# Kernel optimization log

Measured on AMD Instinct MI355X. Metric: run time of the kernel, lower is better.

The kernel has to match this reference:

```python
import jax, jax.numpy as jnp
import numpy as np

B, S, D = 2, 2048, 1024   # batch, seq, d_model
E, K, H = 8, 4, 1024      # experts, top-k, expert hidden
SH = 2 * H                # shared-expert hidden (n_shared_experts=2)


def setup_inputs() -> dict:
    key = jax.random.key(0)
    ks = jax.random.split(key, 24)
    f = lambda k, shape: jax.random.normal(k, shape, dtype=jnp.float32) * 0.02
    return {
        "x": jax.random.normal(ks[0], (B, S, D), dtype=jnp.float32),
        # Linear(in_features, out_features), stored as [in, out]
        "lin0_w": f(ks[1], (D, D)), "lin0_b": f(ks[2], (D,)),
        "swi1_w1": f(ks[3], (D, D)), "swi1_b1": f(ks[4], (D,)),
        "swi1_w2": f(ks[5], (D, D)), "swi1_b2": f(ks[6], (D,)),
        # MoE router (no bias) + routed experts (SwiGLU FFN, no bias)
        "gate_w": f(ks[7], (E, D)),
        "exp_w1": f(ks[8], (E, D, H)),
        "exp_w3": f(ks[9], (E, D, H)),
        "exp_w2": f(ks[10], (E, H, D)),
        # shared experts fused into one wider SwiGLU MLP (2 shared experts)
        "sh_w1": f(ks[11], (D, SH)),
        "sh_w3": f(ks[12], (D, SH)),
        "sh_w2": f(ks[13], (SH, D)),
        # second Linear + SwiGLU block (num_ff=2)
        "lin1_w": f(ks[14], (D, D)), "lin1_b": f(ks[15], (D,)),
        "swi2_w1": f(ks[16], (D, D)), "swi2_b1": f(ks[17], (D,)),
        "swi2_w2": f(ks[18], (D, D)), "swi2_b2": f(ks[19], (D,)),
    }


def _silu(x):
    return x * jax.nn.sigmoid(x)


def _swiglu(x, w1, b1, w2, b2):
    return _silu(x @ w1 + b1) * (x @ w2 + b2)


def _moe(x, gate_w, exp_w1, exp_w3, exp_w2, sh_w1, sh_w3, sh_w2):
    b, s, d = x.shape
    t = b * s
    xt = x.reshape(t, d)
    # router: softmax scores, greedy top-k, normalized weights (scaling factor = 1)
    scores = jax.nn.softmax(xt @ gate_w.T, axis=-1)          # [T, E]
    topv, topi = jax.lax.top_k(scores, K)                    # [T, K]
    topv = topv / jnp.sum(topv, axis=-1, keepdims=True)
    combine = jnp.zeros((t, E), xt.dtype).at[jnp.arange(t)[:, None], topi].set(topv)  # [T, E]
    # routed experts: SwiGLU FFN per expert, dense-masked combine (same math as dispatch)
    g = _silu(jnp.einsum('td,edh->eth', xt, exp_w1))
    u = jnp.einsum('td,edh->eth', xt, exp_w3)
    yexp = jnp.einsum('eth,ehd->etd', g * u, exp_w2)         # [E, T, D]
    routed = jnp.einsum('te,etd->td', combine, yexp)         # [T, D]
    # shared experts (always on)
    shared = (_silu(xt @ sh_w1) * (xt @ sh_w3)) @ sh_w2      # [T, D]
    return (routed + shared).reshape(b, s, d)


def reference(x, lin0_w, lin0_b, swi1_w1, swi1_b1, swi1_w2, swi1_b2,
              gate_w, exp_w1, exp_w3, exp_w2, sh_w1, sh_w3, sh_w2,
              lin1_w, lin1_b, swi2_w1, swi2_b1, swi2_w2, swi2_b2):
    h = x @ lin0_w + lin0_b
    h = _swiglu(h, swi1_w1, swi1_b1, swi1_w2, swi1_b2)
    h = _moe(h, gate_w, exp_w1, exp_w3, exp_w2, sh_w1, sh_w3, sh_w2)
    h = h @ lin1_w + lin1_b
    h = _swiglu(h, swi2_w1, swi2_b1, swi2_w2, swi2_b2)
    return h
```

## Files before the change

### kernel.cpp

```cpp
#include <hip/hip_runtime.h>
#include <cstdint>
#include <cstddef>

#define T_TOKENS 4096
#define D_MODEL  1024
#define N_EXP    8
#define TOP_K    4
#define H_EXP    1024
#define SH_HID   2048
#define TK       (T_TOKENS*TOP_K)

typedef __bf16 bf16x8 __attribute__((ext_vector_type(8)));
typedef __bf16 bf16x4 __attribute__((ext_vector_type(4)));
typedef float  f32x4  __attribute__((ext_vector_type(4)));

__device__ __forceinline__ float silu_f(float x) {
    return x / (1.0f + expf(-x));
}

__device__ __forceinline__ void gload16(void* lds, const void* g)
{
    __builtin_amdgcn_global_load_lds(
        (const __attribute__((address_space(1))) unsigned int*)g,
        (__attribute__((address_space(3))) unsigned int*)lds,
        16, 0, 0);
}

template<int NT, bool SEG, bool GATHER, bool GLU>
__global__ __launch_bounds__(256)
void gemm_sp(const float* __restrict__ A, int lda,
             const float* __restrict__ W1, const float* __restrict__ W3,
             int64_t w_estride, int ldw,
             const float* __restrict__ bias1, const float* __restrict__ bias2,
             float* __restrict__ C, __bf16* __restrict__ Cb1, int ldc,
             int M, int Kd,
             const int* __restrict__ seg_off,
             const int* __restrict__ gather)
{
    constexpr int BM = 128, BN = 128, BK = 32;
    __shared__ __bf16 Asl[NT][BM * BK];
    __shared__ __bf16 Bsl[NT][BN * BK];

    int m0, m1, e = 0;
    if (SEG) {
        e = blockIdx.z;
        int s0 = seg_off[e], s1 = seg_off[e + 1];
        m0 = s0 + blockIdx.y * BM;
        if (m0 >= s1) return;
        m1 = (m0 + BM < s1) ? (m0 + BM) : s1;
    } else {
        m0 = blockIdx.y * BM;
        m1 = (m0 + BM < M) ? (m0 + BM) : M;
    }
    const int n0 = blockIdx.x * BN;

    const int tid  = threadIdx.x;
    const int lane = tid & 63;
    const int w    = tid >> 6;
    const int wm   = w >> 1, wn = w & 1;
    const int fr   = lane & 15, fq = lane >> 4;

    const float* aP[4]; int aR[4], aQ[4];
#pragma unroll
    for (int i = 0; i < 4; ++i) {
        int Li = tid + 256 * i;
        int r = Li >> 3, q = Li & 7;
        aR[i] = r; aQ[i] = q;
        int grow = m0 + r;
        if (grow > m1 - 1) grow = m1 - 1;
        if (GATHER) grow = gather[grow];
        aP[i] = A + (int64_t)grow * lda + q * 4;
    }

    const int bn  = tid & 127;
    const int bkh = tid >> 7;
    const float* Wsrc; int wcol;
    if (GLU) {
        int cl = n0 + bn;
// ... 121 lines not shown
                }
                if (NT == 3) {
                    a = __builtin_amdgcn_mfma_f32_16x16x32_bf16(af[1], bfr[1][jn], a, 0, 0, 0);
                    a = __builtin_amdgcn_mfma_f32_16x16x32_bf16(af[0], bfr[2][jn], a, 0, 0, 0);
                    a = __builtin_amdgcn_mfma_f32_16x16x32_bf16(af[2], bfr[0][jn], a, 0, 0, 0);
                }
                acc[im][jn] = a;
            }
        }
    }
#undef GLOADS

    if (GLU) {
#pragma unroll
        for (int jn = 0; jn < 4; jn += 2) {
            int gcol = (n0 >> 1) + wn * 32 + (jn >> 1) * 16 + fr;
            float bv1 = bias1 ? bias1[gcol] : 0.f;
            float bv2 = bias2 ? bias2[gcol] : 0.f;
#pragma unroll
            for (int im = 0; im < 4; ++im) {
                f32x4 v1 = acc[im][jn];
                f32x4 v2 = acc[im][jn + 1];
#pragma unroll
                for (int r = 0; r < 4; ++r) {
                    int grow = m0 + wm * 64 + im * 16 + fq * 4 + r;
                    if (grow < m1) {
                        float val = silu_f(v1[r] + bv1) * (v2[r] + bv2);
                        int64_t o = (int64_t)grow * ldc + gcol;
                        C[o] = val;
                        if (Cb1) Cb1[o] = (__bf16)val;
                    }
                }
            }
        }
    } else {
#pragma unroll
        for (int jn = 0; jn < 4; ++jn) {
            int col = n0 + wn * 64 + jn * 16 + fr;
            float bv = bias1 ? bias1[col] : 0.f;
#pragma unroll
            for (int im = 0; im < 4; ++im) {
                f32x4 v = acc[im][jn];
#pragma unroll
                for (int r = 0; r < 4; ++r) {
                    int grow = m0 + wm * 64 + im * 16 + fq * 4 + r;
                    if (grow < m1)
                        C[(int64_t)grow * ldc + col] = v[r] + bv;
                }
            }
        }
    }
}

template<bool SEG, bool GATHER, bool GLU, bool EMITB>
__global__ __launch_bounds__(256)
void gemm_gl(const __bf16* __restrict__ A, int lda,
             const __bf16* __restrict__ W1, const __bf16* __restrict__ W3,
             int64_t w_estride, int ldw,
             const float* __restrict__ bias1, const float* __restrict__ bias2,
             float* __restrict__ C, __bf16* __restrict__ Cb, int ldc,
             int M, int Kd,
             const int* __restrict__ seg_off,
             const int* __restrict__ gather)
{
    constexpr int BK = 32;
    __shared__ __bf16 Asl[2][128 * BK];
    __shared__ __bf16 Bsl[2][128 * BK];

    int m0, m1, e = 0;
    if (SEG) {
        e = blockIdx.z;
        int s0 = seg_off[e], s1 = seg_off[e + 1];
        m0 = s0 + blockIdx.y * 128;
        if (m0 >= s1) return;
        m1 = (m0 + 128 < s1) ? (m0 + 128) : s1;
    } else {
        m0 = blockIdx.y * 128;
        m1 = (m0 + 128 < M) ? (m0 + 128) : M;
    }
    const int n0 = blockIdx.x * 128;

    const int tid  = threadIdx.x;
    const int lane = tid & 63;
    const int w    = tid >> 6;
    const int wm   = w >> 1, wn = w & 1;
    const int fr   = lane & 15, fq = lane >> 4;

    const __bf16* As[2]; const __bf16* Ws[2];
    int ldsOff[2];
#pragma unroll
    for (int i = 0; i < 2; ++i) {
        int L = tid + 256 * i;
        int r = L >> 2, cp = L & 3;
        int cs = cp ^ ((r >> 1) & 3);
        ldsOff[i] = (i * 256 + w * 64) * 8;
        int grow = m0 + r;
        if (grow > m1 - 1) grow = m1 - 1;
        if (GATHER) grow = gather[grow];
        As[i] = A + (int64_t)grow * lda + cs * 8;
        int cl = n0 + r;
        const __bf16* base; int srcrow;
        if (GLU) {
            int B = cl >> 4;
            base = (B & 1) ? W3 : W1;
            srcrow = ((B >> 1) << 4) | (cl & 15);
        } else {
            base = W1; srcrow = cl;
        }
        Ws[i] = base + (int64_t)e * w_estride + (int64_t)srcrow * ldw + cs * 8;
    }

#define STAGE(buf, K0)                                                      \
    do {                                                                    \
        _Pragma("unroll")                                                   \
        for (int i = 0; i < 2; ++i) {                                       \
            gload16(&Asl[buf][ldsOff[i]], As[i] + (K0));                    \
            gload16(&Bsl[buf][ldsOff[i]], Ws[i] + (K0));                    \
        }                                                                   \
    } while (0)

    f32x4 zero4 = {0.f, 0.f, 0.f, 0.f};
    f32x4 acc[4][4];
#pragma unroll
    for (int i = 0; i < 4; ++i)
#pragma unroll
        for (int j = 0; j < 4; ++j) acc[i][j] = zero4;

    const int nk = Kd / BK;
    int cur = 0;
    STAGE(0, 0);
    __syncthreads();

    for (int ks = 0; ks < nk; ++ks) {
        if (ks + 1 < nk) STAGE(cur ^ 1, (ks + 1) * BK);

        bf16x8 bfr[4];
#pragma unroll
        for (int j = 0; j < 4; ++j) {
            int rown = wn * 64 + j * 16 + fr;
            int c = fq ^ ((rown >> 1) & 3);
            bfr[j] = *reinterpret_cast<const bf16x8*>(&Bsl[cur][rown * BK + c * 8]);
        }
#pragma unroll
        for (int im = 0; im < 4; ++im) {
            int rowm = wm * 64 + im * 16 + fr;
            int c = fq ^ ((rowm >> 1) & 3);
            bf16x8 af = *reinterpret_cast<const bf16x8*>(&Asl[cur][rowm * BK + c * 8]);
#pragma unroll
            for (int jn = 0; jn < 4; ++jn)
                acc[im][jn] = __builtin_amdgcn_mfma_f32_16x16x32_bf16(af, bfr[jn], acc[im][jn], 0, 0, 0);
        }
        __syncthreads();
        cur ^= 1;
    }
#undef STAGE

    if (GLU) {
#pragma unroll
        for (int jn = 0; jn < 4; jn += 2) {
            int gcol = (n0 >> 1) + wn * 32 + (jn >> 1) * 16 + fr;
            float bv1 = bias1 ? bias1[gcol] : 0.f;
            float bv2 = bias2 ? bias2[gcol] : 0.f;
#pragma unroll
            for (int im = 0; im < 4; ++im) {
                f32x4 v1 = acc[im][jn];
                f32x4 v2 = acc[im][jn + 1];
#pragma unroll
                for (int r = 0; r < 4; ++r) {
                    int grow = m0 + wm * 64 + im * 16 + fq * 4 + r;
                    if (grow < m1) {
                        float val = silu_f(v1[r] + bv1) * (v2[r] + bv2);
                        int64_t o = (int64_t)grow * ldc + gcol;
                        if (EMITB) Cb[o] = (__bf16)val;
                        else       C[o]  = val;
                    }
                }
            }
        }
    } else {
#pragma unroll
        for (int jn = 0; jn < 4; ++jn) {
            int col = n0 + wn * 64 + jn * 16 + fr;
            float bv = bias1 ? bias1[col] : 0.f;
#pragma unroll
            for (int im = 0; im < 4; ++im) {
                f32x4 v = acc[im][jn];
#pragma unroll
                for (int r = 0; r < 4; ++r) {
                    int grow = m0 + wm * 64 + im * 16 + fq * 4 + r;
                    if (grow < m1) {
                        int64_t o = (int64_t)grow * ldc + col;
                        if (EMITB) Cb[o] = (__bf16)(v[r] + bv);
                        else       C[o]  = v[r] + bv;
                    }
                }
            }
        }
    }
}

template<bool WBF, bool SEG, bool GATHER, bool GLU, bool EMITB>
__global__ __launch_bounds__(256)
void gemm_bb(const __bf16* __restrict__ A, int lda,
             const void* __restrict__ W1v, const void* __restrict__ W3v,
             int64_t w_estride, int ldw,
             const float* __restrict__ bias1, const float* __restrict__ bias2,
             float* __restrict__ C, __bf16* __restrict__ Cb, int ldc,
             int M, int Kd,
             const int* __restrict__ seg_off,
             const int* __restrict__ gather)
{
    constexpr int BK = 32;
    __shared__ __bf16 Asl[128 * BK];
    __shared__ __bf16 Bsl[128 * BK];

    int m0, m1, e = 0;
    if (SEG) {
        e = blockIdx.z;
        int s0 = seg_off[e], s1 = seg_off[e + 1];
        m0 = s0 + blockIdx.y * 128;
        if (m0 >= s1) return;
        m1 = (m0 + 128 < s1) ? (m0 + 128) : s1;
    } else {
        m0 = blockIdx.y * 128;
        m1 = (m0 + 128 < M) ? (m0 + 128) : M;
    }
    const int n0 = blockIdx.x * 128;

    const int tid  = threadIdx.x;
    const int lane = tid & 63;
    const int w    = tid >> 6;
    const int wm   = w >> 1, wn = w & 1;
    const int fr   = lane & 15, fq = lane >> 4;

    int aWr[2]; const __bf16* Ab[2];
#pragma unroll
    for (int i = 0; i < 2; ++i) {
        int L = tid + 256 * i;
        int r = L >> 2, ch = L & 3;
        aWr[i] = r * BK + (ch ^ ((r >> 1) & 3)) * 8;
        int grow = m0 + r;
        if (grow > m1 - 1) grow = m1 - 1;
        if (GATHER) grow = gather[grow];
        Ab[i] = A + (int64_t)grow * lda + ch * 8;
    }

    const int bn  = tid & 127;
    const int bkh = tid >> 7;
    int wcol; const void* Wsel;
    if (GLU) {
        int cl = n0 + bn;
        int B  = cl >> 4;
        Wsel = (B & 1) ? W3v : W1v;
        wcol = ((B >> 1) << 4) | (cl & 15);
    } else {
        Wsel = W1v; wcol = n0 + bn;
    }
    const float* Wbf = (const float*)Wsel + (int64_t)e * w_estride + (int64_t)(bkh * 16) * ldw + wcol;
    int wWrS[2];
#pragma unroll
    for (int c = 0; c < 2; ++c)
        wWrS[c] = bn * BK + ((bkh * 2 + c) ^ ((bn >> 1) & 3)) * 8;

    f32x4 zero4 = {0.f, 0.f, 0.f, 0.f};
    f32x4 acc[4][4];
#pragma unroll
    for (int i = 0; i < 4; ++i)
#pragma unroll
        for (int j = 0; j < 4; ++j) acc[i][j] = zero4;

    bf16x8 areg[2];
    bf16x8 wreg[2];

#define GLOADS(K0)                                                          \
    do {                                                                    \
        areg[0] = *reinterpret_cast<const bf16x8*>(Ab[0] + (K0));           \
        areg[1] = *reinterpret_cast<const bf16x8*>(Ab[1] + (K0));           \
        _Pragma("unroll")                                                   \
        for (int j = 0; j < 16; ++j)                                        \
            wreg[j >> 3][j & 7] = (__bf16)Wbf[(int64_t)((K0) + j) * ldw];   \
    } while (0)

    const int nk = Kd / BK;
    GLOADS(0);

    for (int ks = 0; ks < nk; ++ks) {
        __syncthreads();
        *reinterpret_cast<bf16x8*>(&Asl[aWr[0]]) = areg[0];
        *reinterpret_cast<bf16x8*>(&Asl[aWr[1]]) = areg[1];
        *reinterpret_cast<bf16x8*>(&Bsl[wWrS[0]]) = wreg[0];
        *reinterpret_cast<bf16x8*>(&Bsl[wWrS[1]]) = wreg[1];
        if (ks + 1 < nk) GLOADS((ks + 1) * BK);
        __syncthreads();

        bf16x8 bfr[4];
#pragma unroll
        for (int j = 0; j < 4; ++j) {
            int rown = wn * 64 + j * 16 + fr;
            int c = fq ^ ((rown >> 1) & 3);
            bfr[j] = *reinterpret_cast<const bf16x8*>(&Bsl[rown * BK + c * 8]);
        }
#pragma unroll
        for (int im = 0; im < 4; ++im) {
            int rowm = wm * 64 + im * 16 + fr;
            int c = fq ^ ((rowm >> 1) & 3);
            bf16x8 af = *reinterpret_cast<const bf16x8*>(&Asl[rowm * BK + c * 8]);
#pragma unroll
            for (int jn = 0; jn < 4; ++jn)
                acc[im][jn] = __builtin_amdgcn_mfma_f32_16x16x32_bf16(af, bfr[jn], acc[im][jn], 0, 0, 0);
        }
    }
#undef GLOADS

    if (GLU) {
#pragma unroll
        for (int jn = 0; jn < 4; jn += 2) {
            int gcol = (n0 >> 1) + wn * 32 + (jn >> 1) * 16 + fr;
            float bv1 = bias1 ? bias1[gcol] : 0.f;
            float bv2 = bias2 ? bias2[gcol] : 0.f;
#pragma unroll
            for (int im = 0; im < 4; ++im) {
                f32x4 v1 = acc[im][jn];
                f32x4 v2 = acc[im][jn + 1];
#pragma unroll
                for (int r = 0; r < 4; ++r) {
                    int grow = m0 + wm * 64 + im * 16 + fq * 4 + r;
                    if (grow < m1) {
                        float val = silu_f(v1[r] + bv1) * (v2[r] + bv2);
                        int64_t o = (int64_t)grow * ldc + gcol;
                        if (EMITB) Cb[o] = (__bf16)val;
                        else       C[o]  = val;
                    }
                }
            }
        }
    } else {
#pragma unroll
        for (int jn = 0; jn < 4; ++jn) {
            int col = n0 + wn * 64 + jn * 16 + fr;
            float bv = bias1 ? bias1[col] : 0.f;
#pragma unroll
            for (int im = 0; im < 4; ++im) {
                f32x4 v = acc[im][jn];
#pragma unroll
                for (int r = 0; r < 4; ++r) {
                    int grow = m0 + wm * 64 + im * 16 + fq * 4 + r;
                    if (grow < m1) {
                        int64_t o = (int64_t)grow * ldc + col;
                        if (EMITB) Cb[o] = (__bf16)(v[r] + bv);
                        else       C[o]  = v[r] + bv;
                    }
                }
            }
        }
    }
}

__global__ __launch_bounds__(256)
void f2bT(const float* __restrict__ src, __bf16* __restrict__ dst, int R, int C)
{
    __shared__ float t[32][33];
    const int64_t eoff = (int64_t)blockIdx.z * R * C;
    src += eoff; dst += eoff;
    const int c0 = blockIdx.x * 32, r0 = blockIdx.y * 32;
    const int tx = threadIdx.x & 31, ty = threadIdx.x >> 5;
#pragma unroll
    for (int i = 0; i < 4; ++i) {
        int r = r0 + ty + i * 8;
        t[ty + i * 8][tx] = src[(int64_t)r * C + c0 + tx];
    }
    __syncthreads();
#pragma unroll
    for (int i = 0; i < 4; ++i) {
        int c = c0 + ty + i * 8;
        dst[(int64_t)c * R + r0 + tx] = (__bf16)t[tx][ty + i * 8];
    }
}

__global__ __launch_bounds__(256)
void router_logits(const float* __restrict__ h1, const float* __restrict__ gw,
                   int* __restrict__ topi, float* __restrict__ topw,
                   unsigned char* __restrict__ emask)
{
    const int wave = threadIdx.x >> 6, lane = threadIdx.x & 63;
    const int t = blockIdx.x * 4 + wave;
    const float* x = h1 + (int64_t)t * D_MODEL;
    float part[N_EXP];
#pragma unroll
    for (int e = 0; e < N_EXP; ++e) part[e] = 0.f;
#pragma unroll 4
    for (int i = 0; i < D_MODEL / 64; ++i) {
        int d = lane + 64 * i;
        float xv = x[d];
#pragma unroll
        for (int e = 0; e < N_EXP; ++e)
            part[e] = fmaf(xv, gw[e * D_MODEL + d], part[e]);
    }
#pragma unroll
    for (int m = 32; m > 0; m >>= 1)
#pragma unroll
        for (int e = 0; e < N_EXP; ++e)
            part[e] += __shfl_xor(part[e], m, 64);

    if (lane == 0) {
        float p[N_EXP];
        float mx = -1e30f;
#pragma unroll
        for (int e = 0; e < N_EXP; ++e) mx = part[e] > mx ? part[e] : mx;
        float z = 0.f;
#pragma unroll
        for (int e = 0; e < N_EXP; ++e) { p[e] = expf(part[e] - mx); z += p[e]; }
#pragma unroll
        for (int e = 0; e < N_EXP; ++e) p[e] /= z;
        bool used[N_EXP];
#pragma unroll
        for (int e = 0; e < N_EXP; ++e) used[e] = false;
        int sel[TOP_K]; float sv[TOP_K]; float wsum = 0.f;
        unsigned m8 = 0;
        for (int k = 0; k < TOP_K; ++k) {
            int best = 0; float bvv = -1.f;
            for (int e = 0; e < N_EXP; ++e)
                if (!used[e] && p[e] > bvv) { bvv = p[e]; best = e; }
            used[best] = true; sel[k] = best; sv[k] = bvv; wsum += bvv;
            m8 |= 1u << best;
        }
        for (int k = 0; k < TOP_K; ++k) {
            int idx = t * TOP_K + k;
            topi[idx] = sel[k];
// ... 91 lines not shown
                            [s[k] * (D_MODEL / 4) + threadIdx.x];
            yy[0] = (float)yb[0]; yy[1] = (float)yb[1];
            yy[2] = (float)yb[2]; yy[3] = (float)yb[3];
        } else {
            float4 yf = reinterpret_cast<const float4*>((const float*)yv)
                            [s[k] * (D_MODEL / 4) + threadIdx.x];
            yy[0] = yf.x; yy[1] = yf.y; yy[2] = yf.z; yy[3] = yf.w;
        }
        v.x = fmaf(wgt[k], yy[0], v.x);
        v.y = fmaf(wgt[k], yy[1], v.y);
        v.z = fmaf(wgt[k], yy[2], v.z);
        v.w = fmaf(wgt[k], yy[3], v.w);
    }
    if (h2b) {
        bf16x4 o;
        o[0] = (__bf16)v.x; o[1] = (__bf16)v.y;
        o[2] = (__bf16)v.z; o[3] = (__bf16)v.w;
        reinterpret_cast<bf16x4*>(h2b)[base4] = o;
    } else {
        reinterpret_cast<float4*>(h2)[base4] = v;
    }
}

extern "C" void kernel_launch(void* const* d_in, const int* in_sizes, int n_in,
                              void* d_out, int out_size, void* d_ws, size_t ws_size,
                              hipStream_t stream)
{
    const float* x      = (const float*)d_in[0];
    const float* lin0_w = (const float*)d_in[1];
    const float* lin0_b = (const float*)d_in[2];
    const float* s1w1   = (const float*)d_in[3];
    const float* s1b1   = (const float*)d_in[4];
    const float* s1w2   = (const float*)d_in[5];
    const float* s1b2   = (const float*)d_in[6];
    const float* gate_w = (const float*)d_in[7];
    const float* ew1    = (const float*)d_in[8];
    const float* ew3    = (const float*)d_in[9];
    const float* ew2    = (const float*)d_in[10];
    const float* shw1   = (const float*)d_in[11];
    const float* shw3   = (const float*)d_in[12];
    const float* shw2   = (const float*)d_in[13];
    const float* lin1_w = (const float*)d_in[14];
    const float* lin1_b = (const float*)d_in[15];
    const float* s2w1   = (const float*)d_in[16];
    const float* s2b1   = (const float*)d_in[17];
    const float* s2w2   = (const float*)d_in[18];
    const float* s2b2   = (const float*)d_in[19];
    float* out = (float*)d_out;

    char* ws = (char*)d_ws;
    const size_t MB = 1024 * 1024;
    dim3 blk(256);
    const int64_t ES = (int64_t)D_MODEL * H_EXP;
    const bool full = ws_size >= (size_t)216 * MB;

    float* h0 = (float*)(ws + 0 * MB);
    float* h1 = (float*)(ws + 16 * MB);
    float* h2 = (float*)(ws + 32 * MB);

    if (full) {
        __bf16* yexp_b = (__bf16*)(ws + 48 * MB);
        __bf16* gu_b   = (__bf16*)(ws + 80 * MB);
        __bf16* gsh_b  = gu_b;
        __bf16* h1b    = (__bf16*)(ws + 112 * MB);
        __bf16* h2b    = (__bf16*)(ws + 120 * MB);
        __bf16* h3b    = (__bf16*)(ws + 128 * MB);
        __bf16* e1T = (__bf16*)(ws + 136 * MB);
        __bf16* e3T = (__bf16*)(ws + 152 * MB);
        __bf16* e2T = (__bf16*)(ws + 168 * MB);
        __bf16* s1T = (__bf16*)(ws + 184 * MB);
        __bf16* s3T = (__bf16*)(ws + 188 * MB);
        __bf16* s2T = (__bf16*)(ws + 192 * MB);
        __bf16* l1T = (__bf16*)(ws + 196 * MB);
        __bf16* q1T = (__bf16*)(ws + 198 * MB);
        __bf16* q2T = (__bf16*)(ws + 200 * MB);
        char* sm = ws + 202 * MB;
        int*   topi    = (int*)(sm);
        float* topw    = (float*)(sm + 64 * 1024);
        int*   pose    = (int*)(sm + 128 * 1024);
        int*   slot_of = (int*)(sm + 192 * 1024);
        int*   perm    = (int*)(sm + 256 * 1024);
        int*   bh      = (int*)(sm + 320 * 1024);
        int*   bb      = (int*)(sm + 321 * 1024);
        int*   off     = (int*)(sm + 322 * 1024);
        unsigned char* emask = (unsigned char*)(sm + 323 * 1024);

        f2bT<<<dim3(32, 32, N_EXP), blk, 0, stream>>>(ew1, e1T, D_MODEL, H_EXP);
        f2bT<<<dim3(32, 32, N_EXP), blk, 0, stream>>>(ew3, e3T, D_MODEL, H_EXP);
        f2bT<<<dim3(32, 32, N_EXP), blk, 0, stream>>>(ew2, e2T, H_EXP, D_MODEL);
        f2bT<<<dim3(64, 32, 1), blk, 0, stream>>>(shw1, s1T, D_MODEL, SH_HID);
        f2bT<<<dim3(64, 32, 1), blk, 0, stream>>>(shw3, s3T, D_MODEL, SH_HID);
        f2bT<<<dim3(32, 64, 1), blk, 0, stream>>>(shw2, s2T, SH_HID, D_MODEL);
        f2bT<<<dim3(32, 32, 1), blk, 0, stream>>>(lin1_w, l1T, D_MODEL, D_MODEL);
        f2bT<<<dim3(32, 32, 1), blk, 0, stream>>>(s2w1, q1T, D_MODEL, D_MODEL);
        f2bT<<<dim3(32, 32, 1), blk, 0, stream>>>(s2w2, q2T, D_MODEL, D_MODEL);

        gemm_sp<3, false, false, false><<<dim3(8, 32, 1), blk, 0, stream>>>(
            x, D_MODEL, lin0_w, nullptr, 0, D_MODEL, lin0_b, nullptr,
            h0, nullptr, D_MODEL, T_TOKENS, D_MODEL, nullptr, nullptr);

        gemm_sp<3, false, false, true><<<dim3(16, 32, 1), blk, 0, stream>>>(
            h0, D_MODEL, s1w1, s1w2, 0, D_MODEL, s1b1, s1b2,
            h1, h1b, D_MODEL, T_TOKENS, D_MODEL, nullptr, nullptr);

        router_logits<<<T_TOKENS / 4, blk, 0, stream>>>(h1, gate_w, topi, topw, emask);
        rank_local<<<16, blk, 0, stream>>>(emask, topi, pose, bh);
        scan16<<<1, 64, 0, stream>>>(bh, bb, off);
        rank_final<<<16, blk, 0, stream>>>(topi, pose, bb, off, perm, slot_of);

        gemm_gl<true, true, true, true><<<dim3(16, 128, N_EXP), blk, 0, stream>>>(
            h1b, D_MODEL, e1T, e3T, ES, D_MODEL, nullptr, nullptr,
            nullptr, gu_b, H_EXP, 0, D_MODEL, off, perm);
        gemm_gl<true, false, false, true><<<dim3(8, 128, N_EXP), blk, 0, stream>>>(
            gu_b, H_EXP, e2T, nullptr, ES, H_EXP, nullptr, nullptr,
            nullptr, yexp_b, D_MODEL, 0, H_EXP, off, nullptr);
        gemm_gl<false, false, true, true><<<dim3(32, 32, 1), blk, 0, stream>>>(
            h1b, D_MODEL, s1T, s3T, 0, D_MODEL, nullptr, nullptr,
            nullptr, gsh_b, SH_HID, T_TOKENS, D_MODEL, nullptr, nullptr);
        gemm_gl<false, false, false, false><<<dim3(8, 32, 1), blk, 0, stream>>>(
            gsh_b, SH_HID, s2T, nullptr, 0, SH_HID, nullptr, nullptr,
            h2, nullptr, D_MODEL, T_TOKENS, SH_HID, nullptr, nullptr);

        combine_k<true><<<T_TOKENS, blk, 0, stream>>>(yexp_b, topw, slot_of, h2, h2b);

        gemm_gl<false, false, false, true><<<dim3(8, 32, 1), blk, 0, stream>>>(
            h2b, D_MODEL, l1T, nullptr, 0, D_MODEL, lin1_b, nullptr,
            nullptr, h3b, D_MODEL, T_TOKENS, D_MODEL, nullptr, nullptr);

        gemm_gl<false, false, true, false><<<dim3(16, 32, 1), blk, 0, stream>>>(
            h3b, D_MODEL, q1T, q2T, 0, D_MODEL, s2b1, s2b2,
            out, nullptr, D_MODEL, T_TOKENS, D_MODEL, nullptr, nullptr);
    } else {
        float* yexp  = (float*)(ws + 48 * MB);
        __bf16* gu_b = (__bf16*)(ws + 112 * MB);
        __bf16* gsh_b = gu_b;
        __bf16* h1b  = (__bf16*)(ws + 144 * MB);
        char* sm = ws + 152 * MB;
        int*   topi    = (int*)(sm);
        float* topw    = (float*)(sm + 64 * 1024);
        int*   pose    = (int*)(sm + 128 * 1024);
        int*   slot_of = (int*)(sm + 192 * 1024);
        int*   perm    = (int*)(sm + 256 * 1024);
        int*   bh      = (int*)(sm + 320 * 1024);
        int*   bb      = (int*)(sm + 321 * 1024);
        int*   off     = (int*)(sm + 322 * 1024);
        unsigned char* emask = (unsigned char*)(sm + 323 * 1024);

        gemm_sp<3, false, false, false><<<dim3(8, 32, 1), blk, 0, stream>>>(
            x, D_MODEL, lin0_w, nullptr, 0, D_MODEL, lin0_b, nullptr,
            h0, nullptr, D_MODEL, T_TOKENS, D_MODEL, nullptr, nullptr);
        gemm_sp<3, false, false, true><<<dim3(16, 32, 1), blk, 0, stream>>>(
            h0, D_MODEL, s1w1, s1w2, 0, D_MODEL, s1b1, s1b2,
            h1, h1b, D_MODEL, T_TOKENS, D_MODEL, nullptr, nullptr);

        router_logits<<<T_TOKENS / 4, blk, 0, stream>>>(h1, gate_w, topi, topw, emask);
        rank_local<<<16, blk, 0, stream>>>(emask, topi, pose, bh);
        scan16<<<1, 64, 0, stream>>>(bh, bb, off);
        rank_final<<<16, blk, 0, stream>>>(topi, pose, bb, off, perm, slot_of);

        gemm_bb<false, true, true, true, true><<<dim3(16, 128, N_EXP), blk, 0, stream>>>(
            h1b, D_MODEL, ew1, ew3, ES, H_EXP, nullptr, nullptr,
            nullptr, gu_b, H_EXP, 0, D_MODEL, off, perm);
        gemm_bb<false, true, false, false, false><<<dim3(8, 128, N_EXP), blk, 0, stream>>>(
            gu_b, H_EXP, ew2, nullptr, (int64_t)H_EXP * D_MODEL, D_MODEL, nullptr, nullptr,
            yexp, nullptr, D_MODEL, 0, H_EXP, off, nullptr);
        gemm_bb<false, false, false, true, true><<<dim3(32, 32, 1), blk, 0, stream>>>(
            h1b, D_MODEL, shw1, shw3, 0, SH_HID, nullptr, nullptr,
            nullptr, gsh_b, SH_HID, T_TOKENS, D_MODEL, nullptr, nullptr);
        gemm_bb<false, false, false, false, false><<<dim3(8, 32, 1), blk, 0, stream>>>(
            gsh_b, SH_HID, shw2, nullptr, 0, D_MODEL, nullptr, nullptr,
            h2, nullptr, D_MODEL, T_TOKENS, SH_HID, nullptr, nullptr);

        combine_k<false><<<T_TOKENS, blk, 0, stream>>>(yexp, topw, slot_of, h2, nullptr);

        gemm_sp<2, false, false, false><<<dim3(8, 32, 1), blk, 0, stream>>>(
            h2, D_MODEL, lin1_w, nullptr, 0, D_MODEL, lin1_b, nullptr,
            h0, nullptr, D_MODEL, T_TOKENS, D_MODEL, nullptr, nullptr);
        gemm_sp<2, false, false, true><<<dim3(16, 32, 1), blk, 0, stream>>>(
            h0, D_MODEL, s2w1, s2w2, 0, D_MODEL, s2b1, s2b2,
            out, nullptr, D_MODEL, T_TOKENS, D_MODEL, nullptr, nullptr);
    }
}
```

Measured before the change: 609.6 us.

## Replace fp32 first-stage GEMMs with bf16x3 split MFMA GEMMs, drop LDS async loads

The first two GEMMs (lin0 and the first SwiGLU) move from the fp32 gemm_sp path to a new gemm_pl kernel. It splits activations and weights into three bf16 parts and runs six bf16 MFMAs per product to emulate fp32 accuracy. New xsplit3 and f2bT3 kernels produce the split operands, and the lin0 epilogue emits its output already split. Separately, the global_load_lds double-buffered gemm_gl is removed and the later GEMMs use gemm_bb with register-staged single-buffer loads. This risks lower overlap and adds extra split/transpose passes and memory traffic.

```diff
diff --git a/kernel.cpp b/kernel.cpp
--- a/kernel.cpp
+++ b/kernel.cpp
@@ -16,14 +16,6 @@
 
 __device__ __forceinline__ float silu_f(float x) {
     return x / (1.0f + expf(-x));
-}
-
-__device__ __forceinline__ void gload16(void* lds, const void* g)
-{
-    __builtin_amdgcn_global_load_lds(
-        (const __attribute__((address_space(1))) unsigned int*)g,
-        (__attribute__((address_space(3))) unsigned int*)lds,
-        16, 0, 0);
 }
 
 template<int NT, bool SEG, bool GATHER, bool GLU>
@@ -251,10 +243,186 @@
     }
 }
 
-template<bool SEG, bool GATHER, bool GLU, bool EMITB>
+template<bool GLU, int EP>
 __global__ __launch_bounds__(256)
-void gemm_gl(const __bf16* __restrict__ A, int lda,
-             const __bf16* __restrict__ W1, const __bf16* __restrict__ W3,
+void gemm_pl(const __bf16* __restrict__ A0, const __bf16* __restrict__ A1,
+             const __bf16* __restrict__ A2, int lda,
+             const __bf16* __restrict__ W10, const __bf16* __restrict__ W11,
+             const __bf16* __restrict__ W12,
+             const __bf16* __restrict__ W30, const __bf16* __restrict__ W31,
+             const __bf16* __restrict__ W32, int ldw,
+             const float* __restrict__ bias1, const float* __restrict__ bias2,
+             float* __restrict__ C, __bf16* __restrict__ Cb,
+             __bf16* __restrict__ P0, __bf16* __restrict__ P1,
+             __bf16* __restrict__ P2,
+             int ldc, int M, int Kd)
+{
+    constexpr int BK = 32;
+    __shared__ __bf16 Asl[3][128 * BK];
+    __shared__ __bf16 Bsl[3][128 * BK];
+
+    const int m0 = blockIdx.y * 128;
+    const int m1 = (m0 + 128 < M) ? (m0 + 128) : M;
+    const int n0 = blockIdx.x * 128;
+
+    const int tid  = threadIdx.x;
+    const int lane = tid & 63;
+    const int w    = tid >> 6;
+    const int wm   = w >> 1, wn = w & 1;
+    const int fr   = lane & 15, fq = lane >> 4;
+
+    const __bf16* Ap[3] = {A0, A1, A2};
+    const __bf16* W1p[3] = {W10, W11, W12};
+    const __bf16* W3p[3] = {W30, W31, W32};
+
+    int sWr[2];
+    const __bf16* Ab[3][2];
+    const __bf16* Wb[3][2];
+#pragma unroll
+    for (int i = 0; i < 2; ++i) {
+        int L = tid + 256 * i;
+        int r = L >> 2, ch = L & 3;
+        sWr[i] = r * BK + (ch ^ ((r >> 1) & 3)) * 8;
+        int grow = m0 + r;
+        if (grow > m1 - 1) grow = m1 - 1;
+        int cl = n0 + r;
+        int srcrow; bool useW3 = false;
+        if (GLU) {
+            int B = cl >> 4;
+            useW3 = (B & 1);
+            srcrow = ((B >> 1) << 4) | (cl & 15);
+        } else {
+            srcrow = cl;
+        }
+#pragma unroll
+        for (int p = 0; p < 3; ++p) {
+            Ab[p][i] = Ap[p] + (int64_t)grow * lda + ch * 8;
+            const __bf16* base = useW3 ? W3p[p] : W1p[p];
+            Wb[p][i] = base + (int64_t)srcrow * ldw + ch * 8;
+        }
+    }
+
+    f32x4 zero4 = {0.f, 0.f, 0.f, 0.f};
+    f32x4 acc[4][4];
+#pragma unroll
+    for (int i = 0; i < 4; ++i)
+#pragma unroll
+        for (int j = 0; j < 4; ++j) acc[i][j] = zero4;
+
+    bf16x8 areg[3][2];
+    bf16x8 wreg[3][2];
+
+#define GLOADS(K0)                                                          \
+    do {                                                                    \
+        _Pragma("unroll")                                                   \
+        for (int p = 0; p < 3; ++p)                                         \
+            _Pragma("unroll")                                               \
+            for (int i = 0; i < 2; ++i) {                                   \
+                areg[p][i] = *reinterpret_cast<const bf16x8*>(Ab[p][i] + (K0)); \
+                wreg[p][i] = *reinterpret_cast<const bf16x8*>(Wb[p][i] + (K0)); \
+            }                                                               \
+    } while (0)
+
+    const int nk = Kd / BK;
+    GLOADS(0);
+
+    for (int ks = 0; ks < nk; ++ks) {
+        __syncthreads();
+#pragma unroll
+        for (int p = 0; p < 3; ++p)
+#pragma unroll
+            for (int i = 0; i < 2; ++i) {
+                *reinterpret_cast<bf16x8*>(&Asl[p][sWr[i]]) = areg[p][i];
+                *reinterpret_cast<bf16x8*>(&Bsl[p][sWr[i]]) = wreg[p][i];
+            }
+        if (ks + 1 < nk) GLOADS((ks + 1) * BK);
+        __syncthreads();
+
+        bf16x8 bfr[3][4];
+#pragma unroll
+        for (int p = 0; p < 3; ++p)
+#pragma unroll
+            for (int j = 0; j < 4; ++j) {
+                int rown = wn * 64 + j * 16 + fr;
+                int c = fq ^ ((rown >> 1) & 3);
+                bfr[p][j] = *reinterpret_cast<const bf16x8*>(&Bsl[p][rown * BK + c * 8]);
+            }
+#pragma unroll
+        for (int im = 0; im < 4; ++im) {
+            bf16x8 af[3];
+            int rowm = wm * 64 + im * 16 + fr;
+            int c = fq ^ ((rowm >> 1) & 3);
+#pragma unroll
+            for (int p = 0; p < 3; ++p)
+                af[p] = *reinterpret_cast<const bf16x8*>(&Asl[p][rowm * BK + c * 8]);
+#pragma unroll
+            for (int jn = 0; jn < 4; ++jn) {
+                f32x4 a = acc[im][jn];
+                a = __builtin_amdgcn_mfma_f32_16x16x32_bf16(af[0], bfr[0][jn], a, 0, 0, 0);
+                a = __builtin_amdgcn_mfma_f32_16x16x32_bf16(af[0], bfr[1][jn], a, 0, 0, 0);
+                a = __builtin_amdgcn_mfma_f32_16x16x32_bf16(af[1], bfr[0][jn], a, 0, 0, 0);
+                a = __builtin_amdgcn_mfma_f32_16x16x32_bf16(af[1], bfr[1][jn], a, 0, 0, 0);
+                a = __builtin_amdgcn_mfma_f32_16x16x32_bf16(af[0], bfr[2][jn], a, 0, 0, 0);
+                a = __builtin_amdgcn_mfma_f32_16x16x32_bf16(af[2], bfr[0][jn], a, 0, 0, 0);
+                acc[im][jn] = a;
+            }
+        }
+    }
+#undef GLOADS
+
+    if (EP == 1) {
+#pragma unroll
+        for (int jn = 0; jn < 4; jn += 2) {
+            int gcol = (n0 >> 1) + wn * 32 + (jn >> 1) * 16 + fr;
+            float bv1 = bias1 ? bias1[gcol] : 0.f;
+            float bv2 = bias2 ? bias2[gcol] : 0.f;
+#pragma unroll
+            for (int im = 0; im < 4; ++im) {
+                f32x4 v1 = acc[im][jn];
+                f32x4 v2 = acc[im][jn + 1];
+#pragma unroll
+                for (int r = 0; r < 4; ++r) {
+                    int grow = m0 + wm * 64 + im * 16 + fq * 4 + r;
+                    if (grow < m1) {
+                        float val = silu_f(v1[r] + bv1) * (v2[r] + bv2);
+                        int64_t o = (int64_t)grow * ldc + gcol;
+                        C[o]  = val;
+                        Cb[o] = (__bf16)val;
+                    }
+                }
+            }
+        }
+    } else {
+#pragma unroll
+        for (int jn = 0; jn < 4; ++jn) {
+            int col = n0 + wn * 64 + jn * 16 + fr;
+            float bv = bias1 ? bias1[col] : 0.f;
+#pragma unroll
+            for (int im = 0; im < 4; ++im) {
+                f32x4 v = acc[im][jn];
+#pragma unroll
+                for (int r = 0; r < 4; ++r) {
+                    int grow = m0 + wm * 64 + im * 16 + fq * 4 + r;
+                    if (grow < m1) {
+                        float val = v[r] + bv;
+                        int64_t o = (int64_t)grow * ldc + col;
+                        __bf16 h = (__bf16)val;
+                        float  rr = val - (float)h;
+                        __bf16 mm = (__bf16)rr;
+                        P0[o] = h;
+                        P1[o] = mm;
+                        P2[o] = (__bf16)(rr - (float)mm);
+                    }
+                }
+            }
+        }
+    }
+}
+
+template<bool WBF, bool SEG, bool GATHER, bool GLU, bool EMITB>
+__global__ __launch_bounds__(256)
+void gemm_bb(const __bf16* __restrict__ A, int lda,
+             const void* __restrict__ W1v, const void* __restrict__ W3v,
              int64_t w_estride, int ldw,
              const float* __restrict__ bias1, const float* __restrict__ bias2,
              float* __restrict__ C, __bf16* __restrict__ Cb, int ldc,
@@ -263,8 +431,8 @@
              const int* __restrict__ gather)
 {
     constexpr int BK = 32;
-    __shared__ __bf16 Asl[2][128 * BK];
-    __shared__ __bf16 Bsl[2][128 * BK];
+    __shared__ __bf16 Asl[128 * BK];
+    __shared__ __bf16 Bsl[128 * BK];
 
     int m0, m1, e = 0;
     if (SEG) {
@@ -285,74 +453,117 @@
     const int wm   = w >> 1, wn = w & 1;
     const int fr   = lane & 15, fq = lane >> 4;
 
-    const __bf16* As[2]; const __bf16* Ws[2];
-    int ldsOff[2];
+    int aWr[2]; const __bf16* Ab[2];
 #pragma unroll
     for (int i = 0; i < 2; ++i) {
         int L = tid + 256 * i;
-        int r = L >> 2, cp = L & 3;
-        int cs = cp ^ ((r >> 1) & 3);
-        ldsOff[i] = (i * 256 + w * 64) * 8;
+        int r = L >> 2, ch = L & 3;
+        aWr[i] = r * BK + (ch ^ ((r >> 1) & 3)) * 8;
         int grow = m0 + r;
         if (grow > m1 - 1) grow = m1 - 1;
         if (GATHER) grow = gather[grow];
-        As[i] = A + (int64_t)grow * lda + cs * 8;
-        int cl = n0 + r;
-        const __bf16* base; int srcrow;
+        Ab[i] = A + (int64_t)grow * lda + ch * 8;
+    }
+
+    int wR[2]; const __bf16* Wt[2];
+    const float* Wbf = nullptr;
+    int wWrS[2];
+    if (WBF) {
+#pragma unroll
+        for (int i = 0; i < 2; ++i) {
+            int L = tid + 256 * i;
+            int nl = L >> 2, ch = L & 3;
+            wR[i] = nl * BK + (ch ^ ((nl >> 1) & 3)) * 8;
+            int cl = n0 + nl;
+            const __bf16* base;
+            int srcrow;
+            if (GLU) {
+                int B = cl >> 4;
+                base = (const __bf16*)((B & 1) ? W3v : W1v);
+                srcrow = ((B >> 1) << 4) | (cl & 15);
+            } else {
+                base = (const __bf16*)W1v;
+                srcrow = cl;
+            }
+            Wt[i] = base + (int64_t)e * w_estride + (int64_t)srcrow * ldw + ch * 8;
+        }
+    } else {
+        const int bn  = tid & 127;
+        const int bkh = tid >> 7;
+        int wcol; const void* Wsel;
         if (GLU) {
-            int B = cl >> 4;
-            base = (B & 1) ? W3 : W1;
-            srcrow = ((B >> 1) << 4) | (cl & 15);
+            int cl = n0 + bn;
+            int B  = cl >> 4;
+            Wsel = (B & 1) ? W3v : W1v;
+            wcol = ((B >> 1) << 4) | (cl & 15);
         } else {
-            base = W1; srcrow = cl;
-        }
-        Ws[i] = base + (int64_t)e * w_estride + (int64_t)srcrow * ldw + cs * 8;
-    }
-
-#define STAGE(buf, K0)                                                      \
+            Wsel = W1v; wcol = n0 + bn;
+        }
+        Wbf = (const float*)Wsel + (int64_t)e * w_estride + (int64_t)(bkh * 16) * ldw + wcol;
+#pragma unroll
+        for (int c = 0; c < 2; ++c)
+            wWrS[c] = bn * BK + ((bkh * 2 + c) ^ ((bn >> 1) & 3)) * 8;
+    }
+
+    f32x4 zero4 = {0.f, 0.f, 0.f, 0.f};
+    f32x4 acc[4][4];
+#pragma unroll
+    for (int i = 0; i < 4; ++i)
+#pragma unroll
+        for (int j = 0; j < 4; ++j) acc[i][j] = zero4;
+
+    bf16x8 areg[2];
+    bf16x8 wreg[2];
+
+#define GLOADS(K0)                                                          \
     do {                                                                    \
-        _Pragma("unroll")                                                   \
-        for (int i = 0; i < 2; ++i) {                                       \
-            gload16(&Asl[buf][ldsOff[i]], As[i] + (K0));                    \
-            gload16(&Bsl[buf][ldsOff[i]], Ws[i] + (K0));                    \
+        areg[0] = *reinterpret_cast<const bf16x8*>(Ab[0] + (K0));           \
+        areg[1] = *reinterpret_cast<const bf16x8*>(Ab[1] + (K0));           \
+        if (WBF) {                                                          \
+            wreg[0] = *reinterpret_cast<const bf16x8*>(Wt[0] + (K0));       \
+            wreg[1] = *reinterpret_cast<const bf16x8*>(Wt[1] + (K0));       \
+        } else {                                                            \
+            _Pragma("unroll")                                               \
+            for (int j = 0; j < 16; ++j)                                    \
+                wreg[j >> 3][j & 7] = (__bf16)Wbf[(int64_t)((K0) + j) * ldw]; \
         }                                                                   \
     } while (0)
 
-    f32x4 zero4 = {0.f, 0.f, 0.f, 0.f};
-    f32x4 acc[4][4];
-#pragma unroll
-    for (int i = 0; i < 4; ++i)
-#pragma unroll
-        for (int j = 0; j < 4; ++j) acc[i][j] = zero4;
-
     const int nk = Kd / BK;
-    int cur = 0;
-    STAGE(0, 0);
-    __syncthreads();
+    GLOADS(0);
 
     for (int ks = 0; ks < nk; ++ks) {
-        if (ks + 1 < nk) STAGE(cur ^ 1, (ks + 1) * BK);
+        __syncthreads();
+        *reinterpret_cast<bf16x8*>(&Asl[aWr[0]]) = areg[0];
+        *reinterpret_cast<bf16x8*>(&Asl[aWr[1]]) = areg[1];
+        if (WBF) {
+            *reinterpret_cast<bf16x8*>(&Bsl[wR[0]]) = wreg[0];
+            *reinterpret_cast<bf16x8*>(&Bsl[wR[1]]) = wreg[1];
+        } else {
+            *reinterpret_cast<bf16x8*>(&Bsl[wWrS[0]]) = wreg[0];
+            *reinterpret_cast<bf16x8*>(&Bsl[wWrS[1]]) = wreg[1];
+        }
+        if (ks + 1 < nk) GLOADS((ks + 1) * BK);
+        __syncthreads();
 
         bf16x8 bfr[4];
 #pragma unroll
         for (int j = 0; j < 4; ++j) {
             int rown = wn * 64 + j * 16 + fr;
             int c = fq ^ ((rown >> 1) & 3);
-            bfr[j] = *reinterpret_cast<const bf16x8*>(&Bsl[cur][rown * BK + c * 8]);
+            bfr[j] = *reinterpret_cast<const bf16x8*>(&Bsl[rown * BK + c * 8]);
         }
 #pragma unroll
         for (int im = 0; im < 4; ++im) {
             int rowm = wm * 64 + im * 16 + fr;
             int c = fq ^ ((rowm >> 1) & 3);
-            bf16x8 af = *reinterpret_cast<const bf16x8*>(&Asl[cur][rowm * BK + c * 8]);
+            bf16x8 af = *reinterpret_cast<const bf16x8*>(&Asl[rowm * BK + c * 8]);
 #pragma unroll
             for (int jn = 0; jn < 4; ++jn)
                 acc[im][jn] = __builtin_amdgcn_mfma_f32_16x16x32_bf16(af, bfr[jn], acc[im][jn], 0, 0, 0);
         }
-        __syncthreads();
-        cur ^= 1;
-    }
-#undef STAGE
+    }
+#undef GLOADS
 
     if (GLU) {
 #pragma unroll
@@ -398,163 +609,6 @@
     }
 }
 
-template<bool WBF, bool SEG, bool GATHER, bool GLU, bool EMITB>
-__global__ __launch_bounds__(256)
-void gemm_bb(const __bf16* __restrict__ A, int lda,
-             const void* __restrict__ W1v, const void* __restrict__ W3v,
-             int64_t w_estride, int ldw,
-             const float* __restrict__ bias1, const float* __restrict__ bias2,
-             float* __restrict__ C, __bf16* __restrict__ Cb, int ldc,
-             int M, int Kd,
-             const int* __restrict__ seg_off,
-             const int* __restrict__ gather)
-{
-    constexpr int BK = 32;
-    __shared__ __bf16 Asl[128 * BK];
-    __shared__ __bf16 Bsl[128 * BK];
-
-    int m0, m1, e = 0;
-    if (SEG) {
-        e = blockIdx.z;
-        int s0 = seg_off[e], s1 = seg_off[e + 1];
-        m0 = s0 + blockIdx.y * 128;
-        if (m0 >= s1) return;
-        m1 = (m0 + 128 < s1) ? (m0 + 128) : s1;
-    } else {
-        m0 = blockIdx.y * 128;
-        m1 = (m0 + 128 < M) ? (m0 + 128) : M;
-    }
-    const int n0 = blockIdx.x * 128;
-
-    const int tid  = threadIdx.x;
-    const int lane = tid & 63;
-    const int w    = tid >> 6;
-    const int wm   = w >> 1, wn = w & 1;
-    const int fr   = lane & 15, fq = lane >> 4;
-
-    int aWr[2]; const __bf16* Ab[2];
-#pragma unroll
-    for (int i = 0; i < 2; ++i) {
-        int L = tid + 256 * i;
-        int r = L >> 2, ch = L & 3;
-        aWr[i] = r * BK + (ch ^ ((r >> 1) & 3)) * 8;
-        int grow = m0 + r;
-        if (grow > m1 - 1) grow = m1 - 1;
-        if (GATHER) grow = gather[grow];
-        Ab[i] = A + (int64_t)grow * lda + ch * 8;
-    }
-
-    const int bn  = tid & 127;
-    const int bkh = tid >> 7;
-    int wcol; const void* Wsel;
-    if (GLU) {
-        int cl = n0 + bn;
-        int B  = cl >> 4;
-        Wsel = (B & 1) ? W3v : W1v;
-        wcol = ((B >> 1) << 4) | (cl & 15);
-    } else {
-        Wsel = W1v; wcol = n0 + bn;
-    }
-    const float* Wbf = (const float*)Wsel + (int64_t)e * w_estride + (int64_t)(bkh * 16) * ldw + wcol;
-    int wWrS[2];
-#pragma unroll
-    for (int c = 0; c < 2; ++c)
-        wWrS[c] = bn * BK + ((bkh * 2 + c) ^ ((bn >> 1) & 3)) * 8;
-
-    f32x4 zero4 = {0.f, 0.f, 0.f, 0.f};
-    f32x4 acc[4][4];
-#pragma unroll
-    for (int i = 0; i < 4; ++i)
-#pragma unroll
-        for (int j = 0; j < 4; ++j) acc[i][j] = zero4;
-
-    bf16x8 areg[2];
-    bf16x8 wreg[2];
-
-#define GLOADS(K0)                                                          \
-    do {                                                                    \
-        areg[0] = *reinterpret_cast<const bf16x8*>(Ab[0] + (K0));           \
-        areg[1] = *reinterpret_cast<const bf16x8*>(Ab[1] + (K0));           \
-        _Pragma("unroll")                                                   \
-        for (int j = 0; j < 16; ++j)                                        \
-            wreg[j >> 3][j & 7] = (__bf16)Wbf[(int64_t)((K0) + j) * ldw];   \
-    } while (0)
-
-    const int nk = Kd / BK;
-    GLOADS(0);
-
-    for (int ks = 0; ks < nk; ++ks) {
-        __syncthreads();
-        *reinterpret_cast<bf16x8*>(&Asl[aWr[0]]) = areg[0];
-        *reinterpret_cast<bf16x8*>(&Asl[aWr[1]]) = areg[1];
-        *reinterpret_cast<bf16x8*>(&Bsl[wWrS[0]]) = wreg[0];
-        *reinterpret_cast<bf16x8*>(&Bsl[wWrS[1]]) = wreg[1];
-        if (ks + 1 < nk) GLOADS((ks + 1) * BK);
-        __syncthreads();
-
-        bf16x8 bfr[4];
-#pragma unroll
-        for (int j = 0; j < 4; ++j) {
-            int rown = wn * 64 + j * 16 + fr;
-            int c = fq ^ ((rown >> 1) & 3);
-            bfr[j] = *reinterpret_cast<const bf16x8*>(&Bsl[rown * BK + c * 8]);
-        }
-#pragma unroll
-        for (int im = 0; im < 4; ++im) {
-            int rowm = wm * 64 + im * 16 + fr;
-            int c = fq ^ ((rowm >> 1) & 3);
-            bf16x8 af = *reinterpret_cast<const bf16x8*>(&Asl[rowm * BK + c * 8]);
-#pragma unroll
-            for (int jn = 0; jn < 4; ++jn)
-                acc[im][jn] = __builtin_amdgcn_mfma_f32_16x16x32_bf16(af, bfr[jn], acc[im][jn], 0, 0, 0);
-        }
-    }
-#undef GLOADS
-
-    if (GLU) {
-#pragma unroll
-        for (int jn = 0; jn < 4; jn += 2) {
-            int gcol = (n0 >> 1) + wn * 32 + (jn >> 1) * 16 + fr;
-            float bv1 = bias1 ? bias1[gcol] : 0.f;
-            float bv2 = bias2 ? bias2[gcol] : 0.f;
-#pragma unroll
-            for (int im = 0; im < 4; ++im) {
-                f32x4 v1 = acc[im][jn];
-                f32x4 v2 = acc[im][jn + 1];
-#pragma unroll
-                for (int r = 0; r < 4; ++r) {
-                    int grow = m0 + wm * 64 + im * 16 + fq * 4 + r;
-                    if (grow < m1) {
-                        float val = silu_f(v1[r] + bv1) * (v2[r] + bv2);
-                        int64_t o = (int64_t)grow * ldc + gcol;
-                        if (EMITB) Cb[o] = (__bf16)val;
-                        else       C[o]  = val;
-                    }
-                }
-            }
-        }
-    } else {
-#pragma unroll
-        for (int jn = 0; jn < 4; ++jn) {
-            int col = n0 + wn * 64 + jn * 16 + fr;
-            float bv = bias1 ? bias1[col] : 0.f;
-#pragma unroll
-            for (int im = 0; im < 4; ++im) {
-                f32x4 v = acc[im][jn];
-#pragma unroll
-                for (int r = 0; r < 4; ++r) {
-                    int grow = m0 + wm * 64 + im * 16 + fq * 4 + r;
-                    if (grow < m1) {
-                        int64_t o = (int64_t)grow * ldc + col;
-                        if (EMITB) Cb[o] = (__bf16)(v[r] + bv);
-                        else       C[o]  = v[r] + bv;
-                    }
-                }
-            }
-        }
-    }
-}
-
 __global__ __launch_bounds__(256)
 void f2bT(const float* __restrict__ src, __bf16* __restrict__ dst, int R, int C)
 {
@@ -573,6 +627,59 @@
     for (int i = 0; i < 4; ++i) {
         int c = c0 + ty + i * 8;
         dst[(int64_t)c * R + r0 + tx] = (__bf16)t[tx][ty + i * 8];
+    }
+}
+
+__global__ __launch_bounds__(256)
+void f2bT3(const float* __restrict__ src, __bf16* __restrict__ d0,
+           __bf16* __restrict__ d1, __bf16* __restrict__ d2, int R, int C)
+{
+    __shared__ float t[32][33];
+    const int c0 = blockIdx.x * 32, r0 = blockIdx.y * 32;
+    const int tx = threadIdx.x & 31, ty = threadIdx.x >> 5;
+#pragma unroll
+    for (int i = 0; i < 4; ++i) {
+        int r = r0 + ty + i * 8;
+        t[ty + i * 8][tx] = src[(int64_t)r * C + c0 + tx];
+    }
+    __syncthreads();
+#pragma unroll
+    for (int i = 0; i < 4; ++i) {
+        int c = c0 + ty + i * 8;
+        float v = t[tx][ty + i * 8];
+        __bf16 h = (__bf16)v;
+        float  rr = v - (float)h;
+        __bf16 m = (__bf16)rr;
+        int64_t o = (int64_t)c * R + r0 + tx;
+        d0[o] = h;
+        d1[o] = m;
+        d2[o] = (__bf16)(rr - (float)m);
+    }
+}
+
+__global__ void xsplit3(const float* __restrict__ src,
+                        __bf16* __restrict__ p0, __bf16* __restrict__ p1,
+                        __bf16* __restrict__ p2, int64_t n4)
+{
+    int64_t i = (int64_t)blockIdx.x * blockDim.x + threadIdx.x;
+    int64_t st = (int64_t)gridDim.x * blockDim.x;
+    for (; i < n4; i += st) {
+        float4 v = reinterpret_cast<const float4*>(src)[i];
+        float vv[4] = {v.x, v.y, v.z, v.w};
+        bf16x4 a, b, c;
+#pragma unroll
+        for (int t = 0; t < 4; ++t) {
+            float x = vv[t];
+            __bf16 h = (__bf16)x;
+            float  r = x - (float)h;
+            __bf16 m = (__bf16)r;
+            a[t] = h;
+            b[t] = m;
+            c[t] = (__bf16)(r - (float)m);
+        }
+        reinterpret_cast<bf16x4*>(p0)[i] = a;
+        reinterpret_cast<bf16x4*>(p1)[i] = b;
+        reinterpret_cast<bf16x4*>(p2)[i] = c;
     }
 }
 
@@ -770,29 +877,43 @@
     const size_t MB = 1024 * 1024;
     dim3 blk(256);
     const int64_t ES = (int64_t)D_MODEL * H_EXP;
+    const int64_t TD = (int64_t)T_TOKENS * D_MODEL;
     const bool full = ws_size >= (size_t)216 * MB;
 
-    float* h0 = (float*)(ws + 0 * MB);
-    float* h1 = (float*)(ws + 16 * MB);
-    float* h2 = (float*)(ws + 32 * MB);
-
     if (full) {
-        __bf16* yexp_b = (__bf16*)(ws + 48 * MB);
-        __bf16* gu_b   = (__bf16*)(ws + 80 * MB);
+        float*  h1     = (float*) (ws + 0 * MB);
+        float*  h2     = (float*) (ws + 16 * MB);
+        __bf16* yexp_b = (__bf16*)(ws + 32 * MB);
+        __bf16* gu_b   = (__bf16*)(ws + 64 * MB);
         __bf16* gsh_b  = gu_b;
-        __bf16* h1b    = (__bf16*)(ws + 112 * MB);
-        __bf16* h2b    = (__bf16*)(ws + 120 * MB);
-        __bf16* h3b    = (__bf16*)(ws + 128 * MB);
-        __bf16* e1T = (__bf16*)(ws + 136 * MB);
-        __bf16* e3T = (__bf16*)(ws + 152 * MB);
-        __bf16* e2T = (__bf16*)(ws + 168 * MB);
-        __bf16* s1T = (__bf16*)(ws + 184 * MB);
-        __bf16* s3T = (__bf16*)(ws + 188 * MB);
-        __bf16* s2T = (__bf16*)(ws + 192 * MB);
-        __bf16* l1T = (__bf16*)(ws + 196 * MB);
-        __bf16* q1T = (__bf16*)(ws + 198 * MB);
-        __bf16* q2T = (__bf16*)(ws + 200 * MB);
-        char* sm = ws + 202 * MB;
+        __bf16* h1b    = (__bf16*)(ws + 96 * MB);
+        __bf16* h2b    = (__bf16*)(ws + 104 * MB);
+        __bf16* h3b    = (__bf16*)(ws + 112 * MB);
+        __bf16* e1T = (__bf16*)(ws + 120 * MB);
+        __bf16* e3T = (__bf16*)(ws + 136 * MB);
+        __bf16* e2T = (__bf16*)(ws + 152 * MB);
+        __bf16* s1T = (__bf16*)(ws + 168 * MB);
+        __bf16* s3T = (__bf16*)(ws + 172 * MB);
+        __bf16* s2T = (__bf16*)(ws + 176 * MB);
+        __bf16* l1T = (__bf16*)(ws + 180 * MB);
+        __bf16* q1T = (__bf16*)(ws + 182 * MB);
+        __bf16* q2T = (__bf16*)(ws + 184 * MB);
+        __bf16* xp0  = (__bf16*)(ws + 32 * MB);
+        __bf16* xp1  = (__bf16*)(ws + 40 * MB);
+        __bf16* xp2  = (__bf16*)(ws + 48 * MB);
+        __bf16* h0p0 = (__bf16*)(ws + 56 * MB);
+        __bf16* h0p1 = (__bf16*)(ws + 64 * MB);
+        __bf16* h0p2 = (__bf16*)(ws + 72 * MB);
+        __bf16* l0T0 = (__bf16*)(ws + 80 * MB);
+        __bf16* l0T1 = (__bf16*)(ws + 82 * MB);
+        __bf16* l0T2 = (__bf16*)(ws + 84 * MB);
+        __bf16* w1T0 = (__bf16*)(ws + 86 * MB);
+        __bf16* w1T1 = (__bf16*)(ws + 88 * MB);
+        __bf16* w1T2 = (__bf16*)(ws + 90 * MB);
+        __bf16* w3T0 = (__bf16*)(ws + 104 * MB);
+        __bf16* w3T1 = (__bf16*)(ws + 106 * MB);
+        __bf16* w3T2 = (__bf16*)(ws + 108 * MB);
+        char* sm = ws + 186 * MB;
         int*   topi    = (int*)(sm);
         float* topw    = (float*)(sm + 64 * 1024);
         int*   pose    = (int*)(sm + 128 * 1024);
@@ -803,6 +924,10 @@
         int*   off     = (int*)(sm + 322 * 1024);
         unsigned char* emask = (unsigned char*)(sm + 323 * 1024);
 
+        xsplit3<<<2048, blk, 0, stream>>>(x, xp0, xp1, xp2, TD / 4);
+        f2bT3<<<dim3(32, 32, 1), blk, 0, stream>>>(lin0_w, l0T0, l0T1, l0T2, D_MODEL, D_MODEL);
+        f2bT3<<<dim3(32, 32, 1), blk, 0, stream>>>(s1w1, w1T0, w1T1, w1T2, D_MODEL, D_MODEL);
+        f2bT3<<<dim3(32, 32, 1), blk, 0, stream>>>(s1w2, w3T0, w3T1, w3T2, D_MODEL, D_MODEL);
         f2bT<<<dim3(32, 32, N_EXP), blk, 0, stream>>>(ew1, e1T, D_MODEL, H_EXP);
         f2bT<<<dim3(32, 32, N_EXP), blk, 0, stream>>>(ew3, e3T, D_MODEL, H_EXP);
         f2bT<<<dim3(32, 32, N_EXP), blk, 0, stream>>>(ew2, e2T, H_EXP, D_MODEL);
@@ -813,42 +938,48 @@
         f2bT<<<dim3(32, 32, 1), blk, 0, stream>>>(s2w1, q1T, D_MODEL, D_MODEL);
         f2bT<<<dim3(32, 32, 1), blk, 0, stream>>>(s2w2, q2T, D_MODEL, D_MODEL);
 
-        gemm_sp<3, false, false, false><<<dim3(8, 32, 1), blk, 0, stream>>>(
-            x, D_MODEL, lin0_w, nullptr, 0, D_MODEL, lin0_b, nullptr,
-            h0, nullptr, D_MODEL, T_TOKENS, D_MODEL, nullptr, nullptr);
-
-        gemm_sp<3, false, false, true><<<dim3(16, 32, 1), blk, 0, stream>>>(
-            h0, D_MODEL, s1w1, s1w2, 0, D_MODEL, s1b1, s1b2,
-            h1, h1b, D_MODEL, T_TOKENS, D_MODEL, nullptr, nullptr);
+        gemm_pl<false, 2><<<dim3(8, 32, 1), blk, 0, stream>>>(
+            xp0, xp1, xp2, D_MODEL,
+            l0T0, l0T1, l0T2, nullptr, nullptr, nullptr, D_MODEL,
+            lin0_b, nullptr, nullptr, nullptr, h0p0, h0p1, h0p2,
+            D_MODEL, T_TOKENS, D_MODEL);
+
+        gemm_pl<true, 1><<<dim3(16, 32, 1), blk, 0, stream>>>(
+            h0p0, h0p1, h0p2, D_MODEL,
+            w1T0, w1T1, w1T2, w3T0, w3T1, w3T2, D_MODEL,
+            s1b1, s1b2, h1, h1b, nullptr, nullptr, nullptr,
+            D_MODEL, T_TOKENS, D_MODEL);
 
         router_logits<<<T_TOKENS / 4, blk, 0, stream>>>(h1, gate_w, topi, topw, emask);
         rank_local<<<16, blk, 0, stream>>>(emask, topi, pose, bh);
         scan16<<<1, 64, 0, stream>>>(bh, bb, off);
         rank_final<<<16, blk, 0, stream>>>(topi, pose, bb, off, perm, slot_of);
 
-        gemm_gl<true, true, true, true><<<dim3(16, 128, N_EXP), blk, 0, stream>>>(
+        gemm_bb<true, true, true, true, true><<<dim3(16, 128, N_EXP), blk, 0, stream>>>(
             h1b, D_MODEL, e1T, e3T, ES, D_MODEL, nullptr, nullptr,
             nullptr, gu_b, H_EXP, 0, D_MODEL, off, perm);
-        gemm_gl<true, false, false, true><<<dim3(8, 128, N_EXP), blk, 0, stream>>>(
+        gemm_bb<true, true, false, false, true><<<dim3(8, 128, N_EXP), blk, 0, stream>>>(
             gu_b, H_EXP, e2T, nullptr, ES, H_EXP, nullptr, nullptr,
             nullptr, yexp_b, D_MODEL, 0, H_EXP, off, nullptr);
-        gemm_gl<false, false, true, true><<<dim3(32, 32, 1), blk, 0, stream>>>(
+        gemm_bb<true, false, false, true, true><<<dim3(32, 32, 1), blk, 0, stream>>>(
             h1b, D_MODEL, s1T, s3T, 0, D_MODEL, nullptr, nullptr,
             nullptr, gsh_b, SH_HID, T_TOKENS, D_MODEL, nullptr, nullptr);
-        gemm_gl<false, false, false, false><<<dim3(8, 32, 1), blk, 0, stream>>>(
+        gemm_bb<true, false, false, false, false><<<dim3(8, 32, 1), blk, 0, stream>>>(
             gsh_b, SH_HID, s2T, nullptr, 0, SH_HID, nullptr, nullptr,
             h2, nullptr, D_MODEL, T_TOKENS, SH_HID, nullptr, nullptr);
 
         combine_k<true><<<T_TOKENS, blk, 0, stream>>>(yexp_b, topw, slot_of, h2, h2b);
 
-        gemm_gl<false, false, false, true><<<dim3(8, 32, 1), blk, 0, stream>>>(
+        gemm_bb<true, false, false, false, true><<<dim3(8, 32, 1), blk, 0, stream>>>(
             h2b, D_MODEL, l1T, nullptr, 0, D_MODEL, lin1_b, nullptr,
             nullptr, h3b, D_MODEL, T_TOKENS, D_MODEL, nullptr, nullptr);
-
-        gemm_gl<false, false, true, false><<<dim3(16, 32, 1), blk, 0, stream>>>(
+        gemm_bb<true, false, false, true, false><<<dim3(16, 32, 1), blk, 0, stream>>>(
             h3b, D_MODEL, q1T, q2T, 0, D_MODEL, s2b1, s2b2,
             out, nullptr, D_MODEL, T_TOKENS, D_MODEL, nullptr, nullptr);
     } else {
+        float* h0 = (float*)(ws + 0 * MB);
+        float* h1 = (float*)(ws + 16 * MB);
+        float* h2 = (float*)(ws + 32 * MB);
         float* yexp  = (float*)(ws + 48 * MB);
         __bf16* gu_b = (__bf16*)(ws + 112 * MB);
         __bf16* gsh_b = gu_b;
```

Result: no change. 617.9 us (+1.4%).
